# Kernel tuning notes

Hardware: AMD Instinct MI355X
Metric: run time of the kernel (lower is better)

The kernel has to match this reference:

```python
import jax, jax.numpy as jnp
import numpy as np

DIM = 1024
HEADS = 16
DIM_HEAD = 64
INNER = HEADS * DIM_HEAD  # 1024
N = 1024  # seq len == n_features
B = 8
EPS = 1e-5


def setup_inputs() -> dict:
    key = jax.random.key(0)
    ks = jax.random.split(key, 6)
    x = jax.random.normal(ks[0], (B, N, DIM), dtype=jnp.float32)
    ln_gamma = jnp.ones((DIM,), dtype=jnp.float32)
    ln_beta = jnp.zeros((DIM,), dtype=jnp.float32)
    # torch Linear weight is [out, in]; we store transposed [in, out] for x @ W
    w_qkv = jax.random.normal(ks[1], (DIM, 3 * INNER), dtype=jnp.float32) * (DIM ** -0.5)
    w_out = jax.random.normal(ks[2], (INNER, DIM), dtype=jnp.float32) * (INNER ** -0.5)
    attn_bias = jax.random.normal(ks[3], (1, HEADS, N, N), dtype=jnp.float32) * 0.02
    return {"x": x, "ln_gamma": ln_gamma, "ln_beta": ln_beta,
            "w_qkv": w_qkv, "w_out": w_out, "attn_bias": attn_bias}


def reference(x, ln_gamma, ln_beta, w_qkv, w_out, attn_bias):
    # LayerNorm over last dim
    mu = jnp.mean(x, axis=-1, keepdims=True)
    var = jnp.var(x, axis=-1, keepdims=True)
    xn = (x - mu) * jax.lax.rsqrt(var + EPS) * ln_gamma + ln_beta
    # QKV projection (no bias)
    qkv = xn @ w_qkv  # [b, n, 3*inner]
    q, k, v = jnp.split(qkv, 3, axis=-1)
    def to_heads(t):
        return t.reshape(B, N, HEADS, DIM_HEAD).transpose(0, 2, 1, 3)  # b h n d
    q, k, v = to_heads(q), to_heads(k), to_heads(v)
    scale = DIM_HEAD ** -0.5
    q = q * scale
    sim = jnp.einsum('bhid,bhjd->bhij', q, k) + attn_bias  # [b,h,n,n]
    attn = jax.nn.softmax(sim, axis=-1)
    # dropout p=0.0 -> identity
    out = jnp.einsum('bhij,bhjd->bhid', attn, v)  # [b,h,n,d]
    out = out.transpose(0, 2, 1, 3).reshape(B, N, INNER)  # b n (h d)
    return out @ w_out
```

## Files before the change

kernel.cpp:

```cpp
#include <hip/hip_runtime.h>


#define DIM    1024
#define HEADS  16
#define DHEAD  64
#define INNER  1024
#define SEQ    1024
#define BATCH  8
#define QKV3   3072

typedef __bf16 bf16x8 __attribute__((ext_vector_type(8)));
typedef float f32x4 __attribute__((ext_vector_type(4)));
typedef unsigned short u16x8 __attribute__((ext_vector_type(8)));
typedef unsigned short u16x4 __attribute__((ext_vector_type(4)));

typedef __attribute__((address_space(1))) const unsigned int as1_uint;
typedef __attribute__((address_space(3))) unsigned int as3_uint;

static __device__ inline unsigned short f2bf(float f) {
  unsigned int u = __float_as_uint(f);
  u = (u + 0x7FFFu + ((u >> 16) & 1u)) >> 16;
  return (unsigned short)u;
}

__global__ __launch_bounds__(256) void ln_bf16_kernel(
    const float* __restrict__ x, const float* __restrict__ gamma,
    const float* __restrict__ beta, unsigned short* __restrict__ xn) {
  int row = blockIdx.x;
  int tid = threadIdx.x;
  const float4* xr = reinterpret_cast<const float4*>(x + (size_t)row * DIM);
  float4 v = xr[tid];
  float s = v.x + v.y + v.z + v.w;
  float s2 = v.x * v.x + v.y * v.y + v.z * v.z + v.w * v.w;
#pragma unroll
  for (int m = 32; m; m >>= 1) {
    s += __shfl_xor(s, m, 64);
    s2 += __shfl_xor(s2, m, 64);
  }
  __shared__ float red[2][4];
  int wid = tid >> 6, lane = tid & 63;
  if (lane == 0) { red[0][wid] = s; red[1][wid] = s2; }
  __syncthreads();
  s = red[0][0] + red[0][1] + red[0][2] + red[0][3];
  s2 = red[1][0] + red[1][1] + red[1][2] + red[1][3];
  float mu = s * (1.0f / DIM);
  float var = s2 * (1.0f / DIM) - mu * mu;
  float rstd = rsqrtf(var + 1e-5f);
  float4 g = reinterpret_cast<const float4*>(gamma)[tid];
  float4 b = reinterpret_cast<const float4*>(beta)[tid];
  u16x4 o;
  o[0] = f2bf((v.x - mu) * rstd * g.x + b.x);
  o[1] = f2bf((v.y - mu) * rstd * g.y + b.y);
  o[2] = f2bf((v.z - mu) * rstd * g.z + b.z);
  o[3] = f2bf((v.w - mu) * rstd * g.w + b.w);
  *reinterpret_cast<u16x4*>(xn + (size_t)row * DIM + tid * 4) = o;
}

__global__ __launch_bounds__(256) void transpose_cvt(
    const float* __restrict__ W, unsigned short* __restrict__ Wt, int R, int C) {
  __shared__ float tb[32][33];
  int c0 = blockIdx.x * 32, r0 = blockIdx.y * 32;
  int tx = threadIdx.x, ty = threadIdx.y;
#pragma unroll
  for (int i = 0; i < 4; ++i)
    tb[ty + i * 8][tx] = W[(size_t)(r0 + ty + i * 8) * C + c0 + tx];
  __syncthreads();
#pragma unroll
  for (int i = 0; i < 4; ++i)
    Wt[(size_t)(c0 + ty + i * 8) * R + r0 + tx] = f2bf(tb[tx][ty + i * 8]);
}

template <bool F32OUT>
__global__ __launch_bounds__(256) void gemm_bt(
    const unsigned short* __restrict__ A, const unsigned short* __restrict__ Bt,
    void* __restrict__ Cout, int M, int N, int K) {
  __shared__ unsigned short As[128 * 64];
  __shared__ unsigned short Bs[128 * 64];
  int nb = N >> 7;
  int bm = blockIdx.x / nb, bn = blockIdx.x % nb;
  int tid = threadIdx.x, wid = tid >> 6, lane = tid & 63;
  int wr = wid >> 1, wc = wid & 1;
  int lg = lane >> 4, lr = lane & 15;
  f32x4 acc[4][4] = {};
  const unsigned short* Ablk = A + (size_t)(bm * 128) * K;
  const unsigned short* Bblk = Bt + (size_t)(bn * 128) * K;
  int srow = wid * 32 + (lane >> 3);
  int scol = (lane & 7) * 8;
  for (int kt = 0; kt < K; kt += 64) {
#pragma unroll
    for (int t = 0; t < 4; ++t) {
      int r = srow + t * 8;
      __builtin_amdgcn_global_load_lds(
          (as1_uint*)(Ablk + (size_t)r * K + kt + scol),
          (as3_uint*)(&As[(wid * 32 + t * 8) * 64]), 16, 0, 0);
      __builtin_amdgcn_global_load_lds(
          (as1_uint*)(Bblk + (size_t)r * K + kt + scol),
          (as3_uint*)(&Bs[(wid * 32 + t * 8) * 64]), 16, 0, 0);
    }
    __syncthreads();
#pragma unroll
    for (int kk = 0; kk < 2; ++kk) {
      bf16x8 af[4], bfr[4];
#pragma unroll
      for (int mi = 0; mi < 4; ++mi)
        af[mi] = *reinterpret_cast<const bf16x8*>(
            &As[(wr * 64 + mi * 16 + lr) * 64 + kk * 32 + lg * 8]);
#pragma unroll
      for (int ni = 0; ni < 4; ++ni)
        bfr[ni] = *reinterpret_cast<const bf16x8*>(
            &Bs[(wc * 64 + ni * 16 + lr) * 64 + kk * 32 + lg * 8]);
#pragma unroll
      for (int mi = 0; mi < 4; ++mi)
#pragma unroll
        for (int ni = 0; ni < 4; ++ni)
          acc[mi][ni] = __builtin_amdgcn_mfma_f32_16x16x32_bf16(
              af[mi], bfr[ni], acc[mi][ni], 0, 0, 0);
    }
    __syncthreads();
  }
#pragma unroll
  for (int mi = 0; mi < 4; ++mi) {
    int row = bm * 128 + wr * 64 + mi * 16 + lg * 4;
#pragma unroll
    for (int ni = 0; ni < 4; ++ni) {
      int col = bn * 128 + wc * 64 + ni * 16 + lr;
#pragma unroll
      for (int j = 0; j < 4; ++j) {
        if (F32OUT)
          ((float*)Cout)[(size_t)(row + j) * N + col] = acc[mi][ni][j];
        else
          ((unsigned short*)Cout)[(size_t)(row + j) * N + col] = f2bf(acc[mi][ni][j]);
      }
    }
  }
}

__global__ __launch_bounds__(256) void attn_kernel(
    const unsigned short* __restrict__ qkv, const float* __restrict__ bias,
    unsigned short* __restrict__ aout) {
  int id = blockIdx.x;
  int b = id & 7, qt = (id >> 3) & 7, h = id >> 6;
  int tid = threadIdx.x, wid = tid >> 6, lane = tid & 63;
  int lg = lane >> 4, lr = lane & 15;

  __shared__ unsigned short Ks[64 * 72];
  __shared__ unsigned short Vt[64 * 72];
  __shared__ unsigned short Ps[4][32 * 72];

  const unsigned short* qbase = qkv + (size_t)(b * SEQ) * QKV3;
  const float* biash = bias + (size_t)h * SEQ * SEQ;

  bf16x8 qf[2][2];
  int q0 = qt * 128 + wid * 32;
#pragma unroll
  for (int mi = 0; mi < 2; ++mi)
#pragma unroll
    for (int kk = 0; kk < 2; ++kk)
      qf[mi][kk] = *reinterpret_cast<const bf16x8*>(
          qbase + (size_t)(q0 + mi * 16 + lr) * QKV3 + h * 64 + kk * 32 + lg * 8);

  f32x4 oacc[2][4] = {};
  float mrun[2][4], lrun[2][4];
#pragma unroll
  for (int mi = 0; mi < 2; ++mi)
#pragma unroll
    for (int j = 0; j < 4; ++j) { mrun[mi][j] = -1e30f; lrun[mi][j] = 0.f; }

  for (int t = 0; t < 16; ++t) {
#pragma unroll
    for (int it = 0; it < 2; ++it) {
      int e = tid + it * 256;
      int kr = e >> 3, kc = (e & 7) * 8;
      *reinterpret_cast<u16x8*>(&Ks[kr * 72 + kc]) =
          *reinterpret_cast<const u16x8*>(
              qbase + (size_t)(t * 64 + kr) * QKV3 + INNER + h * 64 + kc);
      int vr = e & 63, vc = (e >> 6) * 8;
      u16x8 vv = *reinterpret_cast<const u16x8*>(
          qbase + (size_t)(t * 64 + vr) * QKV3 + 2 * INNER + h * 64 + vc);
#pragma unroll
      for (int i = 0; i < 8; ++i) Vt[(vc + i) * 72 + vr] = vv[i];
    }
    __syncthreads();

    f32x4 sacc[2][4] = {};
#pragma unroll
    for (int kk = 0; kk < 2; ++kk) {
      bf16x8 bk[4];
#pragma unroll
      for (int ni = 0; ni < 4; ++ni)
        bk[ni] = *reinterpret_cast<const bf16x8*>(
            &Ks[(ni * 16 + lr) * 72 + kk * 32 + lg * 8]);
#pragma unroll
      for (int mi = 0; mi < 2; ++mi)
#pragma unroll
        for (int ni = 0; ni < 4; ++ni)
          sacc[mi][ni] = __builtin_amdgcn_mfma_f32_16x16x32_bf16(
              qf[mi][kk], bk[ni], sacc[mi][ni], 0, 0, 0);
    }

    float p[2][4][4];
    float alpha[2][4];
#pragma unroll
    for (int mi = 0; mi < 2; ++mi) {
#pragma unroll
      for (int j = 0; j < 4; ++j) {
        int qrow = q0 + mi * 16 + lg * 4 + j;
        float sv[4], rmax = -1e30f;
#pragma unroll
        for (int ni = 0; ni < 4; ++ni) {
          int kvcol = t * 64 + ni * 16 + lr;
          float xv = sacc[mi][ni][j] * 0.125f + biash[(size_t)qrow * SEQ + kvcol];
          sv[ni] = xv;
          rmax = fmaxf(rmax, xv);
        }
#pragma unroll
        for (int m = 1; m < 16; m <<= 1) rmax = fmaxf(rmax, __shfl_xor(rmax, m, 64));
        float mnew = fmaxf(mrun[mi][j], rmax);
        float a = __expf(mrun[mi][j] - mnew);
        mrun[mi][j] = mnew;
        alpha[mi][j] = a;
        float ls = 0.f;
#pragma unroll
        for (int ni = 0; ni < 4; ++ni) {
          float e = __expf(sv[ni] - mnew);
          p[mi][ni][j] = e;
          ls += e;
        }
#pragma unroll
        for (int m = 1; m < 16; m <<= 1) ls += __shfl_xor(ls, m, 64);
        lrun[mi][j] = lrun[mi][j] * a + ls;
      }
    }

#pragma unroll
    for (int mi = 0; mi < 2; ++mi)
#pragma unroll
      for (int ni = 0; ni < 4; ++ni)
#pragma unroll
        for (int j = 0; j < 4; ++j) {
          oacc[mi][ni][j] *= alpha[mi][j];
          Ps[wid][(mi * 16 + lg * 4 + j) * 72 + ni * 16 + lr] = f2bf(p[mi][ni][j]);
        }

    asm volatile("s_waitcnt lgkmcnt(0)" ::: "memory");

#pragma unroll
    for (int kk = 0; kk < 2; ++kk) {
      bf16x8 pa[2], vb[4];
#pragma unroll
      for (int mi = 0; mi < 2; ++mi)
        pa[mi] = *reinterpret_cast<const bf16x8*>(
            &Ps[wid][(mi * 16 + lr) * 72 + kk * 32 + lg * 8]);
#pragma unroll
      for (int ni = 0; ni < 4; ++ni)
        vb[ni] = *reinterpret_cast<const bf16x8*>(
            &Vt[(ni * 16 + lr) * 72 + kk * 32 + lg * 8]);
#pragma unroll
      for (int mi = 0; mi < 2; ++mi)
#pragma unroll
        for (int ni = 0; ni < 4; ++ni)
          oacc[mi][ni] = __builtin_amdgcn_mfma_f32_16x16x32_bf16(
              pa[mi], vb[ni], oacc[mi][ni], 0, 0, 0);
    }
    __syncthreads();
  }

#pragma unroll
  for (int mi = 0; mi < 2; ++mi)
#pragma unroll
    for (int j = 0; j < 4; ++j) {
      float inv = 1.0f / lrun[mi][j];
      int n = q0 + mi * 16 + lg * 4 + j;
#pragma unroll
      for (int ni = 0; ni < 4; ++ni) {
        int d = ni * 16 + lr;
        aout[(size_t)(b * SEQ + n) * INNER + h * 64 + d] = f2bf(oacc[mi][ni][j] * inv);
      }
    }
}

extern "C" void kernel_launch(void* const* d_in, const int* in_sizes, int n_in,
                              void* d_out, int out_size, void* d_ws, size_t ws_size,
                              hipStream_t stream) {
  const float* x = (const float*)d_in[0];
  const float* gamma = (const float*)d_in[1];
  const float* beta = (const float*)d_in[2];
  const float* w_qkv = (const float*)d_in[3];
  const float* w_out = (const float*)d_in[4];
  const float* bias = (const float*)d_in[5];

  char* ws = (char*)d_ws;
  unsigned short* xn = (unsigned short*)(ws);
  unsigned short* wqkv_t = (unsigned short*)(ws + 16777216);
  unsigned short* wout_t = (unsigned short*)(ws + 23068672);
  unsigned short* qkvb = (unsigned short*)(ws + 25165824);
  unsigned short* aout = (unsigned short*)(ws + 75497472);
  float* out = (float*)d_out;

  ln_bf16_kernel<<<BATCH * SEQ, 256, 0, stream>>>(x, gamma, beta, xn);
  transpose_cvt<<<dim3(QKV3 / 32, DIM / 32), dim3(32, 8), 0, stream>>>(
      w_qkv, wqkv_t, DIM, QKV3);
  transpose_cvt<<<dim3(DIM / 32, INNER / 32), dim3(32, 8), 0, stream>>>(
      w_out, wout_t, INNER, DIM);
  gemm_bt<false><<<(BATCH * SEQ / 128) * (QKV3 / 128), 256, 0, stream>>>(
      xn, wqkv_t, (void*)qkvb, BATCH * SEQ, QKV3, DIM);
  attn_kernel<<<BATCH * HEADS * (SEQ / 128), 256, 0, stream>>>(qkvb, bias, aout);
  gemm_bt<true><<<(BATCH * SEQ / 128) * (DIM / 128), 256, 0, stream>>>(
      aout, wout_t, d_out, BATCH * SEQ, DIM, INNER);
}
```

Baseline: 374.9 us.

## Restructure attention: transposed S layout, K from global, V prefetch, fold scale into weights

Computes S transposed (K as the A operand) so each lane holds contiguous key columns. This allows vectorized float4 bias loads and cuts the row max and sum reductions to two shuffles. K fragments are read straight from global memory instead of staged through LDS. V for the next tile is prefetched into registers and written into a double-buffered LDS tile, which removes the trailing barrier. The 1/8 query scale is folded into the Q weight conversion, and a hardware bf16 convert replaces the manual rounding. In exchange, K is now read uncoalesced from global memory by every wave, which costs extra global traffic.

```diff
diff --git a/kernel.cpp b/kernel.cpp
--- a/kernel.cpp
+++ b/kernel.cpp
@@ -21,6 +21,10 @@
   unsigned int u = __float_as_uint(f);
   u = (u + 0x7FFFu + ((u >> 16) & 1u)) >> 16;
   return (unsigned short)u;
+}
+static __device__ inline unsigned short f2bf_fast(float f) {
+  __bf16 h = (__bf16)f;
+  return __builtin_bit_cast(unsigned short, h);
 }
 
 __global__ __launch_bounds__(256) void ln_bf16_kernel(
@@ -57,7 +61,8 @@
 }
 
 __global__ __launch_bounds__(256) void transpose_cvt(
-    const float* __restrict__ W, unsigned short* __restrict__ Wt, int R, int C) {
+    const float* __restrict__ W, unsigned short* __restrict__ Wt, int R, int C,
+    int scale_rows) {
   __shared__ float tb[32][33];
   int c0 = blockIdx.x * 32, r0 = blockIdx.y * 32;
   int tx = threadIdx.x, ty = threadIdx.y;
@@ -66,8 +71,12 @@
     tb[ty + i * 8][tx] = W[(size_t)(r0 + ty + i * 8) * C + c0 + tx];
   __syncthreads();
 #pragma unroll
-  for (int i = 0; i < 4; ++i)
-    Wt[(size_t)(c0 + ty + i * 8) * R + r0 + tx] = f2bf(tb[tx][ty + i * 8]);
+  for (int i = 0; i < 4; ++i) {
+    int orow = c0 + ty + i * 8;
+    float v = tb[tx][ty + i * 8];
+    if (orow < scale_rows) v *= 0.125f;
+    Wt[(size_t)orow * R + r0 + tx] = f2bf(v);
+  }
 }
 
 template <bool F32OUT>
@@ -143,140 +152,176 @@
   int tid = threadIdx.x, wid = tid >> 6, lane = tid & 63;
   int lg = lane >> 4, lr = lane & 15;
 
-  __shared__ unsigned short Ks[64 * 72];
-  __shared__ unsigned short Vt[64 * 72];
+  __shared__ unsigned short Vt[2][64 * 72];
   __shared__ unsigned short Ps[4][32 * 72];
 
-  const unsigned short* qbase = qkv + (size_t)(b * SEQ) * QKV3;
+  const unsigned short* qbase = qkv + (size_t)(b * SEQ) * QKV3 + h * 64;
+  const unsigned short* kbase = qbase + INNER;
+  const unsigned short* vbase = qbase + 2 * INNER;
   const float* biash = bias + (size_t)h * SEQ * SEQ;
 
+  int q0 = qt * 128 + wid * 32;
+
   bf16x8 qf[2][2];
-  int q0 = qt * 128 + wid * 32;
 #pragma unroll
   for (int mi = 0; mi < 2; ++mi)
 #pragma unroll
     for (int kk = 0; kk < 2; ++kk)
       qf[mi][kk] = *reinterpret_cast<const bf16x8*>(
-          qbase + (size_t)(q0 + mi * 16 + lr) * QKV3 + h * 64 + kk * 32 + lg * 8);
+          qbase + (size_t)(q0 + mi * 16 + lr) * QKV3 + kk * 32 + lg * 8);
+
+  const float* brow[2];
+#pragma unroll
+  for (int mi = 0; mi < 2; ++mi)
+    brow[mi] = biash + (size_t)(q0 + mi * 16 + lr) * SEQ;
+
+  int vrow = tid & 63;
+  int vchunk = tid >> 6;
+  u16x8 vreg[2];
+#pragma unroll
+  for (int it = 0; it < 2; ++it)
+    vreg[it] = *reinterpret_cast<const u16x8*>(
+        vbase + (size_t)vrow * QKV3 + (vchunk + it * 4) * 8);
 
   f32x4 oacc[2][4] = {};
-  float mrun[2][4], lrun[2][4];
-#pragma unroll
-  for (int mi = 0; mi < 2; ++mi)
-#pragma unroll
-    for (int j = 0; j < 4; ++j) { mrun[mi][j] = -1e30f; lrun[mi][j] = 0.f; }
+  float mrun[2] = {-1e30f, -1e30f}, lrun[2] = {0.f, 0.f};
 
   for (int t = 0; t < 16; ++t) {
-#pragma unroll
-    for (int it = 0; it < 2; ++it) {
-      int e = tid + it * 256;
-      int kr = e >> 3, kc = (e & 7) * 8;
-      *reinterpret_cast<u16x8*>(&Ks[kr * 72 + kc]) =
-          *reinterpret_cast<const u16x8*>(
-              qbase + (size_t)(t * 64 + kr) * QKV3 + INNER + h * 64 + kc);
-      int vr = e & 63, vc = (e >> 6) * 8;
-      u16x8 vv = *reinterpret_cast<const u16x8*>(
-          qbase + (size_t)(t * 64 + vr) * QKV3 + 2 * INNER + h * 64 + vc);
-#pragma unroll
-      for (int i = 0; i < 8; ++i) Vt[(vc + i) * 72 + vr] = vv[i];
-    }
+    int cur = t & 1;
+#pragma unroll
+    for (int it = 0; it < 2; ++it)
+#pragma unroll
+      for (int i = 0; i < 8; ++i)
+        Vt[cur][((vchunk + it * 4) * 8 + i) * 72 + vrow] = vreg[it][i];
     __syncthreads();
 
-    f32x4 sacc[2][4] = {};
-#pragma unroll
-    for (int kk = 0; kk < 2; ++kk) {
-      bf16x8 bk[4];
-#pragma unroll
-      for (int ni = 0; ni < 4; ++ni)
-        bk[ni] = *reinterpret_cast<const bf16x8*>(
-            &Ks[(ni * 16 + lr) * 72 + kk * 32 + lg * 8]);
+    bf16x8 kf[4][2];
+#pragma unroll
+    for (int kb = 0; kb < 4; ++kb)
+#pragma unroll
+      for (int kk = 0; kk < 2; ++kk)
+        kf[kb][kk] = *reinterpret_cast<const bf16x8*>(
+            kbase + (size_t)(t * 64 + kb * 16 + lr) * QKV3 + kk * 32 + lg * 8);
+
+    f32x4 bv[2][4];
+#pragma unroll
+    for (int mi = 0; mi < 2; ++mi)
+#pragma unroll
+      for (int kb = 0; kb < 4; ++kb)
+        bv[mi][kb] = *reinterpret_cast<const f32x4*>(
+            brow[mi] + t * 64 + kb * 16 + lg * 4);
+
+    if (t < 15) {
+#pragma unroll
+      for (int it = 0; it < 2; ++it)
+        vreg[it] = *reinterpret_cast<const u16x8*>(
+            vbase + (size_t)((t + 1) * 64 + vrow) * QKV3 + (vchunk + it * 4) * 8);
+    }
+
+    f32x4 s[2][4] = {};
+#pragma unroll
+    for (int kk = 0; kk < 2; ++kk)
+#pragma unroll
+      for (int kb = 0; kb < 4; ++kb)
+#pragma unroll
+        for (int mi = 0; mi < 2; ++mi)
+          s[mi][kb] = __builtin_amdgcn_mfma_f32_16x16x32_bf16(
+              kf[kb][kk], qf[mi][kk], s[mi][kb], 0, 0, 0);
+
+#pragma unroll
+    for (int mi = 0; mi < 2; ++mi)
+#pragma unroll
+      for (int kb = 0; kb < 4; ++kb)
+#pragma unroll
+        for (int j = 0; j < 4; ++j)
+          s[mi][kb][j] += bv[mi][kb][j];
+
+    float alpha[2];
+#pragma unroll
+    for (int mi = 0; mi < 2; ++mi) {
+      float t0 = fmaxf(fmaxf(s[mi][0][0], s[mi][0][1]), fmaxf(s[mi][0][2], s[mi][0][3]));
+      float t1 = fmaxf(fmaxf(s[mi][1][0], s[mi][1][1]), fmaxf(s[mi][1][2], s[mi][1][3]));
+      float t2 = fmaxf(fmaxf(s[mi][2][0], s[mi][2][1]), fmaxf(s[mi][2][2], s[mi][2][3]));
+      float t3 = fmaxf(fmaxf(s[mi][3][0], s[mi][3][1]), fmaxf(s[mi][3][2], s[mi][3][3]));
+      float rm = fmaxf(fmaxf(t0, t1), fmaxf(t2, t3));
+      rm = fmaxf(rm, __shfl_xor(rm, 16, 64));
+      rm = fmaxf(rm, __shfl_xor(rm, 32, 64));
+      float mnew = fmaxf(mrun[mi], rm);
+      alpha[mi] = __expf(mrun[mi] - mnew);
+      mrun[mi] = mnew;
+      float ls = 0.f;
+#pragma unroll
+      for (int kb = 0; kb < 4; ++kb) {
+        float e0 = __expf(s[mi][kb][0] - mnew);
+        float e1 = __expf(s[mi][kb][1] - mnew);
+        float e2 = __expf(s[mi][kb][2] - mnew);
+        float e3 = __expf(s[mi][kb][3] - mnew);
+        s[mi][kb][0] = e0; s[mi][kb][1] = e1;
+        s[mi][kb][2] = e2; s[mi][kb][3] = e3;
+        ls += (e0 + e1) + (e2 + e3);
+      }
+      ls += __shfl_xor(ls, 16, 64);
+      ls += __shfl_xor(ls, 32, 64);
+      lrun[mi] = lrun[mi] * alpha[mi] + ls;
+    }
+
+#pragma unroll
+    for (int mi = 0; mi < 2; ++mi)
+#pragma unroll
+      for (int kb = 0; kb < 4; ++kb) {
+        u16x4 pk;
+        pk[0] = f2bf_fast(s[mi][kb][0]);
+        pk[1] = f2bf_fast(s[mi][kb][1]);
+        pk[2] = f2bf_fast(s[mi][kb][2]);
+        pk[3] = f2bf_fast(s[mi][kb][3]);
+        *reinterpret_cast<u16x4*>(
+            &Ps[wid][(mi * 16 + lr) * 72 + kb * 16 + lg * 4]) = pk;
+      }
+    asm volatile("s_waitcnt lgkmcnt(0)" ::: "memory");
+    __builtin_amdgcn_sched_barrier(0);
+
+#pragma unroll
+    for (int mi = 0; mi < 2; ++mi)
+#pragma unroll
+      for (int db = 0; db < 4; ++db)
+#pragma unroll
+        for (int j = 0; j < 4; ++j)
+          oacc[mi][db][j] *= alpha[mi];
+
+#pragma unroll
+    for (int k2 = 0; k2 < 2; ++k2) {
+      bf16x8 va[4], pb[2];
+#pragma unroll
+      for (int db = 0; db < 4; ++db)
+        va[db] = *reinterpret_cast<const bf16x8*>(
+            &Vt[cur][(db * 16 + lr) * 72 + k2 * 32 + lg * 8]);
 #pragma unroll
       for (int mi = 0; mi < 2; ++mi)
-#pragma unroll
-        for (int ni = 0; ni < 4; ++ni)
-          sacc[mi][ni] = __builtin_amdgcn_mfma_f32_16x16x32_bf16(
-              qf[mi][kk], bk[ni], sacc[mi][ni], 0, 0, 0);
-    }
-
-    float p[2][4][4];
-    float alpha[2][4];
-#pragma unroll
-    for (int mi = 0; mi < 2; ++mi) {
-#pragma unroll
-      for (int j = 0; j < 4; ++j) {
-        int qrow = q0 + mi * 16 + lg * 4 + j;
-        float sv[4], rmax = -1e30f;
-#pragma unroll
-        for (int ni = 0; ni < 4; ++ni) {
-          int kvcol = t * 64 + ni * 16 + lr;
-          float xv = sacc[mi][ni][j] * 0.125f + biash[(size_t)qrow * SEQ + kvcol];
-          sv[ni] = xv;
-          rmax = fmaxf(rmax, xv);
-        }
-#pragma unroll
-        for (int m = 1; m < 16; m <<= 1) rmax = fmaxf(rmax, __shfl_xor(rmax, m, 64));
-        float mnew = fmaxf(mrun[mi][j], rmax);
-        float a = __expf(mrun[mi][j] - mnew);
-        mrun[mi][j] = mnew;
-        alpha[mi][j] = a;
-        float ls = 0.f;
-#pragma unroll
-        for (int ni = 0; ni < 4; ++ni) {
-          float e = __expf(sv[ni] - mnew);
-          p[mi][ni][j] = e;
-          ls += e;
-        }
-#pragma unroll
-        for (int m = 1; m < 16; m <<= 1) ls += __shfl_xor(ls, m, 64);
-        lrun[mi][j] = lrun[mi][j] * a + ls;
-      }
-    }
-
-#pragma unroll
-    for (int mi = 0; mi < 2; ++mi)
-#pragma unroll
-      for (int ni = 0; ni < 4; ++ni)
-#pragma unroll
-        for (int j = 0; j < 4; ++j) {
-          oacc[mi][ni][j] *= alpha[mi][j];
-          Ps[wid][(mi * 16 + lg * 4 + j) * 72 + ni * 16 + lr] = f2bf(p[mi][ni][j]);
-        }
-
-    asm volatile("s_waitcnt lgkmcnt(0)" ::: "memory");
-
-#pragma unroll
-    for (int kk = 0; kk < 2; ++kk) {
-      bf16x8 pa[2], vb[4];
+        pb[mi] = *reinterpret_cast<const bf16x8*>(
+            &Ps[wid][(mi * 16 + lr) * 72 + k2 * 32 + lg * 8]);
 #pragma unroll
       for (int mi = 0; mi < 2; ++mi)
-        pa[mi] = *reinterpret_cast<const bf16x8*>(
-            &Ps[wid][(mi * 16 + lr) * 72 + kk * 32 + lg * 8]);
-#pragma unroll
-      for (int ni = 0; ni < 4; ++ni)
-        vb[ni] = *reinterpret_cast<const bf16x8*>(
-            &Vt[(ni * 16 + lr) * 72 + kk * 32 + lg * 8]);
-#pragma unroll
-      for (int mi = 0; mi < 2; ++mi)
-#pragma unroll
-        for (int ni = 0; ni < 4; ++ni)
-          oacc[mi][ni] = __builtin_amdgcn_mfma_f32_16x16x32_bf16(
-              pa[mi], vb[ni], oacc[mi][ni], 0, 0, 0);
-    }
-    __syncthreads();
-  }
-
-#pragma unroll
-  for (int mi = 0; mi < 2; ++mi)
-#pragma unroll
-    for (int j = 0; j < 4; ++j) {
-      float inv = 1.0f / lrun[mi][j];
-      int n = q0 + mi * 16 + lg * 4 + j;
-#pragma unroll
-      for (int ni = 0; ni < 4; ++ni) {
-        int d = ni * 16 + lr;
-        aout[(size_t)(b * SEQ + n) * INNER + h * 64 + d] = f2bf(oacc[mi][ni][j] * inv);
-      }
-    }
+#pragma unroll
+        for (int db = 0; db < 4; ++db)
+          oacc[mi][db] = __builtin_amdgcn_mfma_f32_16x16x32_bf16(
+              va[db], pb[mi], oacc[mi][db], 0, 0, 0);
+    }
+  }
+
+#pragma unroll
+  for (int mi = 0; mi < 2; ++mi) {
+    float inv = 1.0f / lrun[mi];
+    size_t row = (size_t)(b * SEQ + q0 + mi * 16 + lr) * INNER + h * 64;
+#pragma unroll
+    for (int db = 0; db < 4; ++db) {
+      u16x4 o;
+      o[0] = f2bf_fast(oacc[mi][db][0] * inv);
+      o[1] = f2bf_fast(oacc[mi][db][1] * inv);
+      o[2] = f2bf_fast(oacc[mi][db][2] * inv);
+      o[3] = f2bf_fast(oacc[mi][db][3] * inv);
+      *reinterpret_cast<u16x4*>(&aout[row + db * 16 + lg * 4]) = o;
+    }
+  }
 }
 
 extern "C" void kernel_launch(void* const* d_in, const int* in_sizes, int n_in,
@@ -295,13 +340,12 @@
   unsigned short* wout_t = (unsigned short*)(ws + 23068672);
   unsigned short* qkvb = (unsigned short*)(ws + 25165824);
   unsigned short* aout = (unsigned short*)(ws + 75497472);
-  float* out = (float*)d_out;
 
   ln_bf16_kernel<<<BATCH * SEQ, 256, 0, stream>>>(x, gamma, beta, xn);
   transpose_cvt<<<dim3(QKV3 / 32, DIM / 32), dim3(32, 8), 0, stream>>>(
-      w_qkv, wqkv_t, DIM, QKV3);
+      w_qkv, wqkv_t, DIM, QKV3, INNER);
   transpose_cvt<<<dim3(DIM / 32, INNER / 32), dim3(32, 8), 0, stream>>>(
-      w_out, wout_t, INNER, DIM);
+      w_out, wout_t, INNER, DIM, 0);
   gemm_bt<false><<<(BATCH * SEQ / 128) * (QKV3 / 128), 256, 0, stream>>>(
       xn, wqkv_t, (void*)qkvb, BATCH * SEQ, QKV3, DIM);
   attn_kernel<<<BATCH * HEADS * (SEQ / 128), 256, 0, stream>>>(qkvb, bias, aout);
```

Result: slower. 392.7 us (+4.8%).
